# Kernel optimization log

Measured on AMD Instinct MI355X. Metric: run time of the kernel, lower is better.

## Reference

```python
import jax, jax.numpy as jnp
import numpy as np

B, N, F, W = 8, 2048, 128, 64


def setup_inputs() -> dict:
    key = jax.random.key(0)
    k1, k2, k3, k4 = jax.random.split(key, 4)
    x = jax.random.normal(k1, (B, N, F), dtype=jnp.float32)
    adj = jnp.ones((B, N, N), dtype=bool)  # accepted by forward but unused
    w_key = jax.random.normal(k2, (F, W), dtype=jnp.float32) * 0.1
    w_value = jax.random.normal(k3, (F, F), dtype=jnp.float32) * 0.1
    w_query = jax.random.normal(k4, (F, W), dtype=jnp.float32) * 0.1
    return {"x": x, "adj": adj, "w_key": w_key, "w_value": w_value, "w_query": w_query}


def reference(x, adj, w_key, w_value, w_query):
    # keys/queries: [B, N, W]; values: [B, N, F]
    keys = x @ w_key
    querys = x @ w_query
    values = x @ w_value
    # per-batch softmax(Q K^T) over last dim -> [B, N, N]
    scores = jax.nn.softmax(jnp.einsum('bnw,bmw->bnm', querys, keys), axis=-1)
    # original broadcast-multiply-sum is exactly scores @ values
    out = jnp.einsum('bnm,bmf->bnf', scores, values)
    return out
```

## Files before the change

### kernel.cpp

```cpp
#include <hip/hip_runtime.h>
#include <hip/hip_bf16.h>
#include <math.h>

constexpr int B = 8;
constexpr int N = 2048;
constexpr int F = 128;
constexpr int W = 64;

constexpr int TQ = 128;
constexpr int TK = 64;
constexpr int KSPLIT = 4;
constexpr int TILES_PER_SPLIT = (N / TK) / KSPLIT;

typedef short     bf16x8 __attribute__((ext_vector_type(8)));
typedef _Float16  f16x8  __attribute__((ext_vector_type(8)));
typedef float     f32x4  __attribute__((ext_vector_type(4)));
typedef float     f32x16 __attribute__((ext_vector_type(16)));
typedef ushort    u16x8  __attribute__((ext_vector_type(8)));

__device__ inline ushort f2bf(float f) {
  union { float f; uint u; } v; v.f = f;
  uint u = v.u;
  return (ushort)((u + 0x7FFFu + ((u >> 16) & 1u)) >> 16);
}
__device__ inline float bf2f(ushort h) {
  union { uint u; float f; } v; v.u = ((uint)h) << 16;
  return v.f;
}

__device__ inline void lgkm_barrier() {
  asm volatile("s_waitcnt lgkmcnt(0)" ::: "memory");
  __builtin_amdgcn_s_barrier();
}

__global__ __launch_bounds__(256) void prep_w(
    const float* __restrict__ wq, const float* __restrict__ wk,
    const float* __restrict__ wv, _Float16* __restrict__ wt) {
  int gid = blockIdx.x * 256 + threadIdx.x;
  int n = gid >> 4;
  int k0 = (gid & 15) * 8;
  _Float16 t[8];
#pragma unroll
  for (int j = 0; j < 8; ++j) {
    int k = k0 + j;
    float val = (n < 64)  ? wq[k * W + n]
              : (n < 128) ? wk[k * W + (n - 64)]
                          : wv[k * F + (n - 128)];
    t[j] = (_Float16)val;
  }
  *(uint4*)&wt[n * 128 + k0] = *(uint4*)t;
}

constexpr int KP = 136;

__global__ __launch_bounds__(256) void proj_kernel(
    const float* __restrict__ x, const _Float16* __restrict__ wt,
    _Float16* __restrict__ q16, _Float16* __restrict__ k16,
    ushort* __restrict__ vt_ws) {
  __shared__ _Float16 xs[32][KP];

  const int tid  = threadIdx.x;
  const int wid  = tid >> 6;
  const int lane = tid & 63;
  const int lg = lane >> 4, li = lane & 15;
  const int pass = wid >> 1;
  const int rg   = wid & 1;
  const int brow0 = blockIdx.x * 32;
  const int b    = brow0 / N;
  const int nloc = brow0 % N;

  for (int idx = tid; idx < 32 * 128 / 4; idx += 256) {
    int row = idx >> 5, c4 = idx & 31;
    float4 xv = *(const float4*)&x[(size_t)(brow0 + row) * F + c4 * 4];
    _Float16 h[4] = {(_Float16)xv.x, (_Float16)xv.y,
                     (_Float16)xv.z, (_Float16)xv.w};
    *(float2*)&xs[row][c4 * 4] = *(float2*)h;
  }
  __syncthreads();

  f16x8 xa[4];
#pragma unroll
  for (int kk = 0; kk < 4; ++kk)
    xa[kk] = *(const f16x8*)&xs[rg * 16 + li][kk * 32 + lg * 8];

  f32x4 zero = {0.f, 0.f, 0.f, 0.f};
  f32x4 acc[8];
#pragma unroll
  for (int t = 0; t < 8; ++t) acc[t] = zero;

  const _Float16* wb = wt + (size_t)pass * 128 * 128;

  if (pass == 0) {
#pragma unroll
    for (int kk = 0; kk < 4; ++kk)
#pragma unroll
      for (int nt = 0; nt < 8; ++nt) {
        f16x8 bw = *(const f16x8*)&wb[(nt * 16 + li) * 128 + kk * 32 + lg * 8];
        acc[nt] = __builtin_amdgcn_mfma_f32_16x16x32_f16(xa[kk], bw, acc[nt], 0, 0, 0);
      }
#pragma unroll
    for (int nt = 0; nt < 8; ++nt)
#pragma unroll
      for (int r = 0; r < 4; ++r) {
        int row = brow0 + rg * 16 + lg * 4 + r;
        int c = nt * 16 + li;
        _Float16 hv = (_Float16)acc[nt][r];
        if (nt < 4) q16[row * W + c] = hv;
        else        k16[row * W + (c - 64)] = hv;
      }
  } else {
#pragma unroll
    for (int kk = 0; kk < 4; ++kk)
#pragma unroll
      for (int mt = 0; mt < 8; ++mt) {
        f16x8 aw = *(const f16x8*)&wb[(mt * 16 + li) * 128 + kk * 32 + lg * 8];
        acc[mt] = __builtin_amdgcn_mfma_f32_16x16x32_f16(aw, xa[kk], acc[mt], 0, 0, 0);
      }
    const int n   = nloc + rg * 16 + li;
    const int kt  = n >> 6;
    const int kk2 = (n >> 4) & 3;
    const int fl  = ((n >> 3) & 1) * 32;
    const int ei  = n & 7;
    ushort* vb = vt_ws + (((size_t)(b * 32 + kt) * 4 + kk2) * 4) * 512;
#pragma unroll
    for (int mt = 0; mt < 8; ++mt)
#pragma unroll
      for (int r = 0; r < 4; ++r) {
        int f = mt * 16 + lg * 4 + r;
        vb[(size_t)(f >> 5) * 512 + (size_t)(fl + (f & 31)) * 8 + ei] =
            f2bf(acc[mt][r]);
      }
  }
}

constexpr int LK = 72;

__global__ __launch_bounds__(256, 2) void attn_kernel(
    const _Float16* __restrict__ q16, const _Float16* __restrict__ k16,
    const ushort* __restrict__ vfr,
    ushort* __restrict__ op0, ushort* __restrict__ op1,
    ushort* __restrict__ op2, ushort* __restrict__ op3,
    float* __restrict__ lsums) {
  __shared__ _Float16 ksh[2][TK][LK];
  __shared__ ushort  ps[4][32][LK];

  const int tid  = threadIdx.x;
  const int wid  = tid >> 6;
  const int lane = tid & 63;
  const int q32  = lane & 31;
  const int hi   = lane >> 5;

  const int hw    = blockIdx.x;
  const int grp   = (hw & 7) | ((hw >> 7) << 3);
  const int qt    = (hw >> 3) & 15;
  const int b     = grp & 7;
  const int split = grp >> 3;

  const size_t koffb = (size_t)b * N * W;
  const ushort* vfb_base = vfr + (size_t)b * 32 * 16 * 512;

  const size_t qrow = (size_t)(b * N + qt * TQ + wid * 32 + q32) * W + hi * 8;
  f16x8 qa[4];
#pragma unroll
  for (int kk = 0; kk < 4; ++kk)
    qa[kk] = *(const f16x8*)&q16[qrow + kk * 16];

  const int krow0 = tid >> 3, krow1 = krow0 + 32, kc8 = tid & 7;
  uint4 kr0, kr1;
  auto load_k = [&](int kt) {
    kr0 = *(const uint4*)&k16[koffb + ((size_t)kt * TK + krow0) * W + kc8 * 8];
    kr1 = *(const uint4*)&k16[koffb + ((size_t)kt * TK + krow1) * W + kc8 * 8];
  };

  float l_lane = 0.f;
  f32x16 oa[4];
#pragma unroll
  for (int ft = 0; ft < 4; ++ft)
#pragma unroll
    for (int r = 0; r < 16; ++r) oa[ft][r] = 0.f;

  const int kt0 = split * TILES_PER_SPLIT;
  load_k(kt0);

  for (int t = 0; t < TILES_PER_SPLIT; ++t) {
    const int kt = kt0 + t;
    const int pb = t & 1;

    const ushort* vfb = vfb_base + (size_t)kt * 16 * 512 + (size_t)lane * 8;
    uint4 vreg[16];
#pragma unroll
    for (int kk2 = 0; kk2 < 4; ++kk2) {
      const ushort* vb2 = vfb + kk2 * 2048;
      vreg[kk2 * 4 + 0] = *(const uint4*)&vb2[0];
      vreg[kk2 * 4 + 1] = *(const uint4*)&vb2[512];
      vreg[kk2 * 4 + 2] = *(const uint4*)&vb2[1024];
      vreg[kk2 * 4 + 3] = *(const uint4*)&vb2[1536];
    }

    *(uint4*)&ksh[pb][krow0][kc8 * 8] = kr0;
    *(uint4*)&ksh[pb][krow1][kc8 * 8] = kr1;
    if (t + 1 < TILES_PER_SPLIT) load_k(kt + 1);

    lgkm_barrier();

    f32x16 s2[2];
#pragma unroll
    for (int mt = 0; mt < 2; ++mt)
#pragma unroll
      for (int r = 0; r < 16; ++r) s2[mt][r] = 0.f;
#pragma unroll
    for (int kk = 0; kk < 4; ++kk)
#pragma unroll
      for (int mt = 0; mt < 2; ++mt) {
        f16x8 kf = *(const f16x8*)&ksh[pb][mt * 32 + q32][kk * 16 + hi * 8];
        s2[mt] = __builtin_amdgcn_mfma_f32_32x32x16_f16(kf, qa[kk], s2[mt], 0, 0, 0);
      }

#pragma unroll
    for (int mt = 0; mt < 2; ++mt)
#pragma unroll
      for (int gq = 0; gq < 4; ++gq) {
        ushort ph[4];
#pragma unroll
        for (int j = 0; j < 4; ++j) {
          float p = __expf(s2[mt][gq * 4 + j]);
          ph[j] = f2bf(p);
          l_lane += bf2f(ph[j]);
        }
        *(float2*)&ps[wid][q32][mt * 32 + gq * 8 + hi * 4] = *(float2*)ph;
      }

#pragma unroll
    for (int kk2 = 0; kk2 < 4; ++kk2) {
      bf16x8 pa = *(const bf16x8*)&ps[wid][q32][kk2 * 16 + hi * 8];
#pragma unroll
      for (int ft = 0; ft < 4; ++ft) {
        bf16x8 vf = __builtin_bit_cast(bf16x8, vreg[kk2 * 4 + ft]);
        oa[ft] = __builtin_amdgcn_mfma_f32_32x32x16_bf16(pa, vf, oa[ft], 0, 0, 0);
      }
    }
  }

  l_lane += __shfl_xor(l_lane, 32, 64);

  ushort* opb = (split == 0) ? op0 : (split == 1) ? op1 : (split == 2) ? op2 : op3;
  ushort* ob = opb + (size_t)(b * N + qt * TQ + wid * 32) * F;
#pragma unroll
  for (int ft = 0; ft < 4; ++ft)
#pragma unroll
    for (int r = 0; r < 16; ++r) {
      int qr = (r & 3) + 8 * (r >> 2) + 4 * hi;
      ob[(size_t)qr * F + ft * 32 + q32] = f2bf(oa[ft][r]);
    }
  if (hi == 0) {
    size_t gr = (size_t)split * B * N + (size_t)(b * N + qt * TQ) + wid * 32 + q32;
    lsums[gr] = l_lane;
  }
}

__global__ __launch_bounds__(256) void combine_kernel(
    const ushort* __restrict__ op0, const ushort* __restrict__ op1,
    const ushort* __restrict__ op2, const ushort* __restrict__ op3,
    const float* __restrict__ lsums, float* __restrict__ out) {
  const int t  = blockIdx.x * 256 + threadIdx.x;
  const int gr = t >> 4;
  const int c8 = (t & 15) * 8;
  constexpr size_t BN = (size_t)B * N;
  const float l = lsums[gr] + lsums[BN + gr] + lsums[2 * BN + gr] + lsums[3 * BN + gr];
  const float inv = 1.f / l;
  const size_t base = (size_t)gr * F + c8;
  u16x8 a0 = *(const u16x8*)&op0[base];
  u16x8 a1 = *(const u16x8*)&op1[base];
  u16x8 a2 = *(const u16x8*)&op2[base];
  u16x8 a3 = *(const u16x8*)&op3[base];
  float o[8];
#pragma unroll
  for (int j = 0; j < 8; ++j)
    o[j] = (bf2f(a0[j]) + bf2f(a1[j]) + bf2f(a2[j]) + bf2f(a3[j])) * inv;
  *(float4*)&out[base]     = *(float4*)&o[0];
  *(float4*)&out[base + 4] = *(float4*)&o[4];
}

extern "C" void kernel_launch(void* const* d_in, const int* in_sizes, int n_in,
                              void* d_out, int out_size, void* d_ws, size_t ws_size,
                              hipStream_t stream) {
  const float* x  = (const float*)d_in[0];
  const float* wk = (const float*)d_in[2];
  const float* wv = (const float*)d_in[3];
  const float* wq = (const float*)d_in[4];
  float* out = (float*)d_out;

  constexpr size_t BNW = (size_t)B * N * W;
  constexpr size_t BNF = (size_t)B * N * F;
  _Float16* q16 = (_Float16*)d_ws;
  _Float16* k16 = q16 + BNW;
  ushort*   vt  = (ushort*)(k16 + BNW);
  _Float16* wt  = (_Float16*)(vt + BNF);
  ushort*   op0 = (ushort*)(wt + 32768);
  ushort*   op1 = op0 + BNF;
  ushort*   op2 = op1 + BNF;
  ushort*   op3 = op2 + BNF;
  float*    ls  = (float*)(op3 + BNF);

  prep_w<<<16, 256, 0, stream>>>(wq, wk, wv, wt);
  proj_kernel<<<(B * N) / 32, 256, 0, stream>>>(x, wt, q16, k16, vt);
  attn_kernel<<<dim3(512), 256, 0, stream>>>(q16, k16, vt, op0, op1, op2, op3, ls);
  combine_kernel<<<(B * N * F / 8) / 256, 256, 0, stream>>>(op0, op1, op2, op3, ls, out);
}
```

Before: 208.6 us.

## Keep softmax probabilities in registers and permute V layout to match MFMA fragments

Removes the LDS round trip for the probability tile. P values are now packed directly from the QK^T MFMA accumulators with v_cvt_pk_bf16_f32 and used as the A operand of the PV MFMA. To keep this correct, the V transpose layout written by the projection kernel is permuted so the key ordering matches the accumulator row layout. It also adds s_setprio around the MFMA sections and interleaves batch indices across blocks in the proj and combine kernels, which may affect cache and channel locality. Row sums are now taken from fp32 probabilities instead of rounded bf16 values, a small numerical change.

After: 207.3 us (median of 3 runs). No clear change (-0.6%).

```diff
diff --git a/kernel.cpp b/kernel.cpp
--- a/kernel.cpp
+++ b/kernel.cpp
@@ -65,9 +65,10 @@
   const int lg = lane >> 4, li = lane & 15;
   const int pass = wid >> 1;
   const int rg   = wid & 1;
-  const int brow0 = blockIdx.x * 32;
-  const int b    = brow0 / N;
-  const int nloc = brow0 % N;
+  const int bx   = blockIdx.x;
+  const int b    = bx & 7;
+  const int nloc = (bx >> 3) * 32;
+  const int brow0 = b * N + nloc;
 
   for (int idx = tid; idx < 32 * 128 / 4; idx += 256) {
     int row = idx >> 5, c4 = idx & 31;
@@ -119,8 +120,8 @@
     const int n   = nloc + rg * 16 + li;
     const int kt  = n >> 6;
     const int kk2 = (n >> 4) & 3;
-    const int fl  = ((n >> 3) & 1) * 32;
-    const int ei  = n & 7;
+    const int fl  = ((n >> 2) & 1) * 32;
+    const int ei  = (n & 3) + 4 * ((n >> 3) & 1);
     ushort* vb = vt_ws + (((size_t)(b * 32 + kt) * 4 + kk2) * 4) * 512;
 #pragma unroll
     for (int mt = 0; mt < 8; ++mt)
@@ -142,7 +143,6 @@
     ushort* __restrict__ op2, ushort* __restrict__ op3,
     float* __restrict__ lsums) {
   __shared__ _Float16 ksh[2][TK][LK];
-  __shared__ ushort  ps[4][32][LK];
 
   const int tid  = threadIdx.x;
   const int wid  = tid >> 6;
@@ -208,6 +208,7 @@
     for (int mt = 0; mt < 2; ++mt)
 #pragma unroll
       for (int r = 0; r < 16; ++r) s2[mt][r] = 0.f;
+    __builtin_amdgcn_s_setprio(1);
 #pragma unroll
     for (int kk = 0; kk < 4; ++kk)
 #pragma unroll
@@ -215,30 +216,41 @@
         f16x8 kf = *(const f16x8*)&ksh[pb][mt * 32 + q32][kk * 16 + hi * 8];
         s2[mt] = __builtin_amdgcn_mfma_f32_32x32x16_f16(kf, qa[kk], s2[mt], 0, 0, 0);
       }
-
-#pragma unroll
-    for (int mt = 0; mt < 2; ++mt)
-#pragma unroll
-      for (int gq = 0; gq < 4; ++gq) {
-        ushort ph[4];
-#pragma unroll
-        for (int j = 0; j < 4; ++j) {
-          float p = __expf(s2[mt][gq * 4 + j]);
-          ph[j] = f2bf(p);
-          l_lane += bf2f(ph[j]);
-        }
-        *(float2*)&ps[wid][q32][mt * 32 + gq * 8 + hi * 4] = *(float2*)ph;
-      }
-
-#pragma unroll
-    for (int kk2 = 0; kk2 < 4; ++kk2) {
-      bf16x8 pa = *(const bf16x8*)&ps[wid][q32][kk2 * 16 + hi * 8];
+    __builtin_amdgcn_s_setprio(0);
+
+    uint4 paw[4];
+#pragma unroll
+    for (int mt = 0; mt < 2; ++mt) {
+      float pf[16];
+#pragma unroll
+      for (int r = 0; r < 16; ++r) pf[r] = __expf(s2[mt][r]);
+      float t0 = (pf[0] + pf[1]) + (pf[2] + pf[3]);
+      float t1 = (pf[4] + pf[5]) + (pf[6] + pf[7]);
+      float t2 = (pf[8] + pf[9]) + (pf[10] + pf[11]);
+      float t3 = (pf[12] + pf[13]) + (pf[14] + pf[15]);
+      l_lane += (t0 + t1) + (t2 + t3);
+#pragma unroll
+      for (int gm = 0; gm < 2; ++gm) {
+        uint w0, w1, w2, w3;
+        asm("v_cvt_pk_bf16_f32 %0, %1, %2" : "=v"(w0) : "v"(pf[gm * 8 + 0]), "v"(pf[gm * 8 + 1]));
+        asm("v_cvt_pk_bf16_f32 %0, %1, %2" : "=v"(w1) : "v"(pf[gm * 8 + 2]), "v"(pf[gm * 8 + 3]));
+        asm("v_cvt_pk_bf16_f32 %0, %1, %2" : "=v"(w2) : "v"(pf[gm * 8 + 4]), "v"(pf[gm * 8 + 5]));
+        asm("v_cvt_pk_bf16_f32 %0, %1, %2" : "=v"(w3) : "v"(pf[gm * 8 + 6]), "v"(pf[gm * 8 + 7]));
+        paw[mt * 2 + gm] = make_uint4(w0, w1, w2, w3);
+      }
+    }
+
+    __builtin_amdgcn_s_setprio(1);
+#pragma unroll
+    for (int g = 0; g < 4; ++g) {
+      bf16x8 pa = __builtin_bit_cast(bf16x8, paw[g]);
 #pragma unroll
       for (int ft = 0; ft < 4; ++ft) {
-        bf16x8 vf = __builtin_bit_cast(bf16x8, vreg[kk2 * 4 + ft]);
+        bf16x8 vf = __builtin_bit_cast(bf16x8, vreg[g * 4 + ft]);
         oa[ft] = __builtin_amdgcn_mfma_f32_32x32x16_bf16(pa, vf, oa[ft], 0, 0, 0);
       }
     }
+    __builtin_amdgcn_s_setprio(0);
   }
 
   l_lane += __shfl_xor(l_lane, 32, 64);
@@ -262,9 +274,9 @@
     const ushort* __restrict__ op0, const ushort* __restrict__ op1,
     const ushort* __restrict__ op2, const ushort* __restrict__ op3,
     const float* __restrict__ lsums, float* __restrict__ out) {
-  const int t  = blockIdx.x * 256 + threadIdx.x;
-  const int gr = t >> 4;
-  const int c8 = (t & 15) * 8;
+  const int bx = blockIdx.x;
+  const int gr = (bx & 7) * N + (bx >> 3) * 16 + (threadIdx.x >> 4);
+  const int c8 = (threadIdx.x & 15) * 8;
   constexpr size_t BN = (size_t)B * N;
   const float l = lsums[gr] + lsums[BN + gr] + lsums[2 * BN + gr] + lsums[3 * BN + gr];
   const float inv = 1.f / l;
@@ -305,5 +317,5 @@
   prep_w<<<16, 256, 0, stream>>>(wq, wk, wv, wt);
   proj_kernel<<<(B * N) / 32, 256, 0, stream>>>(x, wt, q16, k16, vt);
   attn_kernel<<<dim3(512), 256, 0, stream>>>(q16, k16, vt, op0, op1, op2, op3, ls);
-  combine_kernel<<<(B * N * F / 8) / 256, 256, 0, stream>>>(op0, op1, op2, op3, ls, out);
-}
+  combine_kernel<<<(B * N) / 16, 256, 0, stream>>>(op0, op1, op2, op3, ls, out);
+}
```
